# Kernel tuning notes

Measured on AMD Instinct MI355X. Metric: run time of the kernel, lower is better.

## Reference

```python
import jax, jax.numpy as jnp
import numpy as np

N_EMBD = 2048
N_HEAD = 16
HEAD_DIM = N_EMBD // N_HEAD
MAX_SEQ = 2048
ROPE_BASE = 10000.0


def _build_rope_cache(seq_len, head_dim, base):
    theta = 1.0 / (base ** (jnp.arange(0, head_dim, 2, dtype=jnp.float32) / head_dim))
    idx_theta = jnp.arange(seq_len, dtype=jnp.float32)[:, None] * theta[None, :]  # [T, hd/2]
    return jnp.cos(idx_theta), jnp.sin(idx_theta)


def _apply_rope(x, cos, sin):
    # x: [B, T, H, hd]; interleaved (even, odd) pairing along last dim
    B, T, H, hd = x.shape
    xf = x.astype(jnp.float32).reshape(B, T, H, hd // 2, 2)
    x0, x1 = xf[..., 0], xf[..., 1]
    c = cos[None, :T, None, :]
    s = sin[None, :T, None, :]
    out = jnp.stack([x0 * c - x1 * s, x1 * c + x0 * s], axis=-1)
    return out.reshape(B, T, H, hd).astype(x.dtype)


def setup_inputs() -> dict:
    key = jax.random.key(0)
    k1, k2, k3 = jax.random.split(key, 3)
    x = jax.random.normal(k1, (2, 2048, N_EMBD), dtype=jnp.float32)
    # torch Linear(D, 3D, bias=False): y = x @ W.T ; store as [D, 3D] for x @ W
    scale = 1.0 / np.sqrt(N_EMBD)
    w_attn = jax.random.normal(k2, (N_EMBD, 3 * N_EMBD), dtype=jnp.float32) * scale
    w_proj = jax.random.normal(k3, (N_EMBD, N_EMBD), dtype=jnp.float32) * scale
    return {"x": x, "w_attn": w_attn, "w_proj": w_proj}


def reference(x, w_attn, w_proj):
    B, T, D = x.shape
    cos, sin = _build_rope_cache(MAX_SEQ, HEAD_DIM, ROPE_BASE)
    qkv = x @ w_attn                                   # [B, T, 3D]
    q, k, v = jnp.split(qkv, 3, axis=-1)
    q = q.reshape(B, T, N_HEAD, HEAD_DIM)
    k = k.reshape(B, T, N_HEAD, HEAD_DIM)
    v = v.reshape(B, T, N_HEAD, HEAD_DIM)
    q = _apply_rope(q, cos, sin)
    k = _apply_rope(k, cos, sin)
    # non-causal SDPA (original calls F.sdpa without is_causal)
    scale = 1.0 / jnp.sqrt(jnp.asarray(HEAD_DIM, dtype=q.dtype))
    scores = jnp.einsum("bqhd,bkhd->bhqk", q, k) * scale
    attn = jax.nn.softmax(scores, axis=-1)
    y = jnp.einsum("bhqk,bkhd->bqhd", attn, v).reshape(B, T, D)
    return y @ w_proj
```

## Files before the change

kernel.cpp:

```cpp
#include <hip/hip_runtime.h>
#include <cstdint>
#include <cstddef>

typedef __attribute__((ext_vector_type(8))) short bf16x8;
typedef __attribute__((ext_vector_type(8))) unsigned short us8;
typedef __attribute__((ext_vector_type(4))) float f32x4;

#define TSEQ 2048

__device__ __forceinline__ unsigned short f2bf(float f) {
  union { float f; uint32_t u; } v; v.f = f;
  uint32_t u = v.u;
  uint32_t r = (u + 0x7FFFu + ((u >> 16) & 1u)) >> 16;
  return (unsigned short)r;
}
__device__ __forceinline__ unsigned short f2bf_trunc(float f) {
  union { float f; uint32_t u; } v; v.f = f;
  return (unsigned short)(v.u >> 16);
}
__device__ __forceinline__ float bf2f(unsigned short h) {
  union { uint32_t u; float f; } v; v.u = ((uint32_t)h) << 16;
  return v.f;
}

__device__ __forceinline__ void async16(const void* g, void* l) {
  __builtin_amdgcn_global_load_lds(
      (const __attribute__((address_space(1))) unsigned int*)g,
      (__attribute__((address_space(3))) unsigned int*)l,
      16, 0, 0);
}

__global__ __launch_bounds__(256) void rope_table(float2* __restrict__ tbl)
{
  const int idx = blockIdx.x * 256 + threadIdx.x;
  const int t = idx >> 6;
  const int j = idx & 63;
  float sn, cs;
  sincosf((float)t * exp2f((float)j * -0.2076205059273837f), &sn, &cs);
  tbl[idx] = make_float2(cs, sn);
}

__global__ __launch_bounds__(256) void cvt_x(
    const float* __restrict__ in, unsigned short* __restrict__ out)
{
  const size_t i = ((size_t)blockIdx.x * 256 + threadIdx.x) * 16;
  f32x4 a0 = *(const f32x4*)(in + i);
  f32x4 a1 = *(const f32x4*)(in + i + 4);
  f32x4 a2 = *(const f32x4*)(in + i + 8);
  f32x4 a3 = *(const f32x4*)(in + i + 12);
  us8 lo, hi;
#pragma unroll
  for (int j = 0; j < 4; j++) {
    lo[j] = f2bf(a0[j]); lo[j + 4] = f2bf(a1[j]);
    hi[j] = f2bf(a2[j]); hi[j + 4] = f2bf(a3[j]);
  }
  *(us8*)(out + i) = lo;
  *(us8*)(out + i + 8) = hi;
}

__global__ __launch_bounds__(256) void transpose_w(
    const float* __restrict__ in, unsigned short* __restrict__ out,
    int R, int C)
{
  __shared__ unsigned short tile[32][33];
  const int bx = blockIdx.x * 32;
  const int by = blockIdx.y * 32;
  const int tx = threadIdx.x & 31;
  const int ty = threadIdx.x >> 5;
#pragma unroll
  for (int r = ty; r < 32; r += 8)
    tile[r][tx] = f2bf(in[(size_t)(by + r) * C + bx + tx]);
  __syncthreads();
#pragma unroll
  for (int r = ty; r < 32; r += 8)
    out[(size_t)(bx + r) * R + by + tx] = tile[tx][r];
}

template <int MODE>
__global__ __launch_bounds__(256) void gemm_bt(
    const unsigned short* __restrict__ A,
    const unsigned short* __restrict__ Bt,
    void* __restrict__ Cv,
    int M, int N, int K, int ldc,
    const float2* __restrict__ tbl)
{
  __shared__ unsigned short As[2][128 * 32];
  __shared__ unsigned short Bs[2][128 * 32];
  const int tid  = threadIdx.x;
  const int lane = tid & 63;
  const int w    = tid >> 6;
  const int m0   = blockIdx.y * 128;
  const int n0   = blockIdx.x * 128;
  const int wm   = (w & 1) * 64;
  const int wn   = (w >> 1) * 64;

  const int srow = lane >> 2;
  const int scol = (lane & 3) * 8;
  const unsigned short* ga0 = A  + (size_t)(m0 + w * 16 + srow) * K + scol;
  const unsigned short* ga1 = ga0 + (size_t)64 * K;
  const unsigned short* gb0 = Bt + (size_t)(n0 + w * 16 + srow) * K + scol;
  const unsigned short* gb1 = gb0 + (size_t)64 * K;

  f32x4 acc[4][4];
#pragma unroll
  for (int i = 0; i < 4; i++)
#pragma unroll
    for (int j = 0; j < 4; j++) acc[i][j] = (f32x4){0.f, 0.f, 0.f, 0.f};

  const int frow = lane & 15;
  const int fcol = (lane >> 4) * 8;

  for (int kt = 0; kt < K; kt += 64) {
    __syncthreads();
    async16(ga0 + kt,      &As[0][w * 512]);
    async16(ga1 + kt,      &As[0][(4 + w) * 512]);
    async16(ga0 + kt + 32, &As[1][w * 512]);
    async16(ga1 + kt + 32, &As[1][(4 + w) * 512]);
    async16(gb0 + kt,      &Bs[0][w * 512]);
    async16(gb1 + kt,      &Bs[0][(4 + w) * 512]);
    async16(gb0 + kt + 32, &Bs[1][w * 512]);
    async16(gb1 + kt + 32, &Bs[1][(4 + w) * 512]);
    __syncthreads();

#pragma unroll
    for (int h = 0; h < 2; h++) {
      bf16x8 af[4], bfr[4];
#pragma unroll
      for (int i = 0; i < 4; i++)
        af[i] = *(const bf16x8*)&As[h][(wm + i * 16 + frow) * 32 + fcol];
#pragma unroll
      for (int i = 0; i < 4; i++)
        bfr[i] = *(const bf16x8*)&Bs[h][(wn + i * 16 + frow) * 32 + fcol];
#pragma unroll
      for (int mi = 0; mi < 4; mi++)
#pragma unroll
        for (int ni = 0; ni < 4; ni++)
          acc[mi][ni] = __builtin_amdgcn_mfma_f32_16x16x32_bf16(
              af[mi], bfr[ni], acc[mi][ni], 0, 0, 0);
    }
  }

  const int crow0 = m0 + wm + (lane >> 4) * 4;
  const int ccol0 = n0 + wn + (lane & 15);
  if (MODE == 1) {
    float* Cf = (float*)Cv;
#pragma unroll
    for (int mi = 0; mi < 4; mi++)
#pragma unroll
      for (int i = 0; i < 4; i++) {
        const int row = crow0 + mi * 16 + i;
#pragma unroll
        for (int ni = 0; ni < 4; ni++)
          Cf[(size_t)row * ldc + ccol0 + ni * 16] = acc[mi][ni][i];
      }
  } else {
    unsigned short* Cb = (unsigned short*)Cv;
    const bool doRope = (n0 < 4096);
    const float sc = (n0 < 2048) ? 0.08838834764831845f : 1.0f;
    const int odd = lane & 1;
#pragma unroll
    for (int mi = 0; mi < 4; mi++)
#pragma unroll
      for (int i = 0; i < 4; i++) {
        const int row = crow0 + mi * 16 + i;
        if (doRope) {
          const size_t tof = (size_t)(row & (TSEQ - 1)) * 64;
          float2 cs[4];
#pragma unroll
          for (int ni = 0; ni < 4; ni++)
            cs[ni] = tbl[tof + (((ccol0 + ni * 16) & 126) >> 1)];
#pragma unroll
          for (int ni = 0; ni < 4; ni++) {
            const float v = acc[mi][ni][i];
            const float p = __shfl_xor(v, 1);
            const float o = (odd ? (v * cs[ni].x + p * cs[ni].y)
                                 : (v * cs[ni].x - p * cs[ni].y)) * sc;
            Cb[(size_t)row * ldc + ccol0 + ni * 16] = f2bf(o);
          }
        } else {
#pragma unroll
          for (int ni = 0; ni < 4; ni++)
            Cb[(size_t)row * ldc + ccol0 + ni * 16] = f2bf(acc[mi][ni][i]);
        }
      }
  }
}

__global__ __launch_bounds__(256) void repack_v(
    const unsigned short* __restrict__ qkv, unsigned short* __restrict__ Vtg)
{
  __shared__ unsigned short tile[32][33];
  const int tt = blockIdx.x * 32;
  const int dd = blockIdx.y * 32;
  const int bh = blockIdx.z;
  const int b  = bh >> 4, h = bh & 15;
  const int tx = threadIdx.x & 31;
  const int ty = threadIdx.x >> 5;
#pragma unroll
  for (int r = ty; r < 32; r += 8)
    tile[r][tx] = qkv[(size_t)(b * TSEQ + tt + r) * 6144 + 4096 + h * 128 + dd + tx];
  __syncthreads();
#pragma unroll
  for (int r = ty; r < 32; r += 8)
    Vtg[(size_t)bh * 262144 + (size_t)(dd + r) * TSEQ + tt + tx] = tile[tx][r];
}

__global__ __launch_bounds__(256) void attn(
    const unsigned short* __restrict__ qkv,
    const unsigned short* __restrict__ Vtg,
    unsigned short* __restrict__ y)
{
  __shared__ unsigned short Ks[64 * 136];
  __shared__ unsigned short Vs[128 * 72];
  __shared__ unsigned short Ps[4][32 * 72];

  const int tid  = threadIdx.x;
  const int lane = tid & 63;
  const int w    = tid >> 6;
  const int q0   = blockIdx.x * 128;
  const int h    = blockIdx.y;
  const int b    = blockIdx.z;
  const int bh   = b * 16 + h;
  const int quad = lane >> 4;
  const int l15  = lane & 15;
  const int kq   = quad * 8;

  bf16x8 qa[2][4];
#pragma unroll
  for (int mt = 0; mt < 2; mt++) {
    const unsigned short* gQ =
        qkv + (size_t)(b * TSEQ + q0 + w * 32 + mt * 16 + l15) * 6144 + h * 128 + kq;
#pragma unroll
    for (int dc = 0; dc < 4; dc++) qa[mt][dc] = *(const bf16x8*)(gQ + dc * 32);
  }

  f32x4 ot[2][8];
#pragma unroll
  for (int mt = 0; mt < 2; mt++)
#pragma unroll
    for (int nt = 0; nt < 8; nt++) ot[mt][nt] = (f32x4){0.f, 0.f, 0.f, 0.f};
  float rs[2][4];
#pragma unroll
  for (int mt = 0; mt < 2; mt++)
#pragma unroll
    for (int i = 0; i < 4; i++) rs[mt][i] = 0.f;

  const int krow = tid >> 2;
  const int kd   = (tid & 3) * 32;
  const unsigned short* gK = qkv + (size_t)(b * TSEQ) * 6144 + 2048 + h * 128 + kd;
  const int vd = tid >> 1;
  const int vc = (tid & 1) * 32;
  const unsigned short* gVt = Vtg + (size_t)bh * 262144 + (size_t)vd * TSEQ + vc;

  us8 kreg[4], vreg[4];
  {
    const unsigned short* pk = gK + (size_t)krow * 6144;
#pragma unroll
    for (int j = 0; j < 4; j++) kreg[j] = *(const us8*)(pk + j * 8);
#pragma unroll
    for (int j = 0; j < 4; j++) vreg[j] = *(const us8*)(gVt + j * 8);
  }

  for (int kb = 0; kb < TSEQ; kb += 64) {
    __syncthreads();
#pragma unroll
    for (int j = 0; j < 4; j++)
      *(us8*)&Ks[krow * 136 + kd + j * 8] = kreg[j];
#pragma unroll
    for (int j = 0; j < 4; j++)
      *(us8*)&Vs[vd * 72 + vc + j * 8] = vreg[j];
    __syncthreads();

    if (kb + 64 < TSEQ) {
      const unsigned short* pk = gK + (size_t)(kb + 64 + krow) * 6144;
#pragma unroll
      for (int j = 0; j < 4; j++) kreg[j] = *(const us8*)(pk + j * 8);
      const unsigned short* pv = gVt + kb + 64;
#pragma unroll
      for (int j = 0; j < 4; j++) vreg[j] = *(const us8*)(pv + j * 8);
    }

    f32x4 s[2][4];
#pragma unroll
    for (int mt = 0; mt < 2; mt++)
#pragma unroll
      for (int ct = 0; ct < 4; ct++) s[mt][ct] = (f32x4){0.f, 0.f, 0.f, 0.f};
    __builtin_amdgcn_s_setprio(1);
#pragma unroll
    for (int dc = 0; dc < 4; dc++) {
#pragma unroll
      for (int ct = 0; ct < 4; ct++) {
        bf16x8 kf = *(const bf16x8*)&Ks[(ct * 16 + l15) * 136 + dc * 32 + kq];
        s[0][ct] = __builtin_amdgcn_mfma_f32_16x16x32_bf16(qa[0][dc], kf, s[0][ct], 0, 0, 0);
        s[1][ct] = __builtin_amdgcn_mfma_f32_16x16x32_bf16(qa[1][dc], kf, s[1][ct], 0, 0, 0);
      }
    }
    __builtin_amdgcn_s_setprio(0);

    unsigned short* pw = &Ps[w][0];
    float t8[2][4];
#pragma unroll
    for (int mt = 0; mt < 2; mt++)
#pragma unroll
      for (int i = 0; i < 4; i++) t8[mt][i] = 0.f;
#pragma unroll
    for (int mt = 0; mt < 2; mt++)
#pragma unroll
      for (int ct = 0; ct < 4; ct++)
#pragma unroll
        for (int i = 0; i < 4; i++) {
          const unsigned short us = f2bf_trunc(__expf(fminf(s[mt][ct][i], 30.f)));
          pw[(mt * 16 + quad * 4 + i) * 72 + ct * 16 + l15] = us;
          t8[mt][i] += bf2f(us);
        }
#pragma unroll
    for (int mt = 0; mt < 2; mt++)
#pragma unroll
      for (int i = 0; i < 4; i++) {
        float v = t8[mt][i];
        v += __shfl_xor(v, 1);
        v += __shfl_xor(v, 2);
        v += __shfl_xor(v, 4);
        v += __shfl_xor(v, 8);
        rs[mt][i] += v;
      }

    __asm__ volatile("s_waitcnt lgkmcnt(0)" ::: "memory");

    __builtin_amdgcn_s_setprio(1);
#pragma unroll
    for (int kc = 0; kc < 2; kc++) {
      bf16x8 pa0 = *(const bf16x8*)&pw[(l15) * 72 + kc * 32 + kq];
      bf16x8 pa1 = *(const bf16x8*)&pw[(16 + l15) * 72 + kc * 32 + kq];
#pragma unroll
      for (int nt = 0; nt < 8; nt++) {
        bf16x8 vb = *(const bf16x8*)&Vs[(nt * 16 + l15) * 72 + kc * 32 + kq];
        ot[0][nt] = __builtin_amdgcn_mfma_f32_16x16x32_bf16(pa0, vb, ot[0][nt], 0, 0, 0);
        ot[1][nt] = __builtin_amdgcn_mfma_f32_16x16x32_bf16(pa1, vb, ot[1][nt], 0, 0, 0);
      }
    }
    __builtin_amdgcn_s_setprio(0);
  }

#pragma unroll
  for (int mt = 0; mt < 2; mt++) {
    unsigned short* gy =
        y + (size_t)(b * TSEQ + q0 + w * 32 + mt * 16 + quad * 4) * 2048 + h * 128 + l15;
#pragma unroll
    for (int i = 0; i < 4; i++) {
      const float inv = 1.0f / rs[mt][i];
#pragma unroll
      for (int nt = 0; nt < 8; nt++)
        gy[(size_t)i * 2048 + nt * 16] = f2bf(ot[mt][nt][i] * inv);
    }
  }
}

extern "C" void kernel_launch(void* const* d_in, const int* in_sizes, int n_in,
                              void* d_out, int out_size, void* d_ws, size_t ws_size,
                              hipStream_t stream)
{
  const float* x      = (const float*)d_in[0];
  const float* w_attn = (const float*)d_in[1];
  const float* w_proj = (const float*)d_in[2];

  if (ws_size < 67108864u) return;

  char* ws = (char*)d_ws;
  unsigned short* qkv = (unsigned short*)(ws);
  unsigned short* xb  = (unsigned short*)(ws + 50331648);
  unsigned short* y   = xb;
  unsigned short* wT2 = (unsigned short*)(ws);
  unsigned short* wTa = (unsigned short*)d_out;
  float2* tbl = (float2*)((char*)d_out + 25165824);
  unsigned short* Vtg = (unsigned short*)d_out;

  transpose_w<<<dim3(192, 64), 256, 0, stream>>>(w_attn, wTa, 2048, 6144);
  rope_table<<<dim3(512), 256, 0, stream>>>(tbl);
  cvt_x<<<dim3(2048), 256, 0, stream>>>(x, xb);
  gemm_bt<2><<<dim3(48, 32), 256, 0, stream>>>(xb, wTa, (void*)qkv, 4096, 6144, 2048, 6144, tbl);
  repack_v<<<dim3(64, 4, 32), 256, 0, stream>>>(qkv, Vtg);
  attn<<<dim3(16, 16, 2), 256, 0, stream>>>(qkv, Vtg, y);
  transpose_w<<<dim3(64, 64), 256, 0, stream>>>(w_proj, wT2, 2048, 2048);
  gemm_bt<1><<<dim3(16, 32), 256, 0, stream>>>(y, wT2, d_out, 4096, 2048, 2048, 2048, nullptr);
}
```

Measured before the change: 453.9 us.

## Unfuse RoPE from QKV GEMM epilogue into standalone pass; vectorize V repack

Removes the precomputed rope table and the RoPE/scale epilogue from the QKV GEMM. A separate rope_qk kernel now reads Q and K back from the bf16 buffer, computes sin/cos inline and rewrites them in place. repack_v is rewritten to move 128-bit vectors through a larger padded tile. This simplifies the GEMM epilogue (no table loads or shuffles) at the cost of an extra read-write pass over Q and K, plus a second bf16 rounding before RoPE.

```diff
diff --git a/kernel.cpp b/kernel.cpp
--- a/kernel.cpp
+++ b/kernel.cpp
@@ -28,16 +28,6 @@
       (const __attribute__((address_space(1))) unsigned int*)g,
       (__attribute__((address_space(3))) unsigned int*)l,
       16, 0, 0);
-}
-
-__global__ __launch_bounds__(256) void rope_table(float2* __restrict__ tbl)
-{
-  const int idx = blockIdx.x * 256 + threadIdx.x;
-  const int t = idx >> 6;
-  const int j = idx & 63;
-  float sn, cs;
-  sincosf((float)t * exp2f((float)j * -0.2076205059273837f), &sn, &cs);
-  tbl[idx] = make_float2(cs, sn);
 }
 
 __global__ __launch_bounds__(256) void cvt_x(
@@ -76,13 +66,12 @@
     out[(size_t)(bx + r) * R + by + tx] = tile[tx][r];
 }
 
-template <int MODE>
+template <int CF32>
 __global__ __launch_bounds__(256) void gemm_bt(
     const unsigned short* __restrict__ A,
     const unsigned short* __restrict__ Bt,
     void* __restrict__ Cv,
-    int M, int N, int K, int ldc,
-    const float2* __restrict__ tbl)
+    int M, int N, int K, int ldc)
 {
   __shared__ unsigned short As[2][128 * 32];
   __shared__ unsigned short Bs[2][128 * 32];
@@ -142,7 +131,7 @@
 
   const int crow0 = m0 + wm + (lane >> 4) * 4;
   const int ccol0 = n0 + wn + (lane & 15);
-  if (MODE == 1) {
+  if (CF32) {
     float* Cf = (float*)Cv;
 #pragma unroll
     for (int mi = 0; mi < 4; mi++)
@@ -155,54 +144,75 @@
       }
   } else {
     unsigned short* Cb = (unsigned short*)Cv;
-    const bool doRope = (n0 < 4096);
-    const float sc = (n0 < 2048) ? 0.08838834764831845f : 1.0f;
-    const int odd = lane & 1;
 #pragma unroll
     for (int mi = 0; mi < 4; mi++)
 #pragma unroll
       for (int i = 0; i < 4; i++) {
         const int row = crow0 + mi * 16 + i;
-        if (doRope) {
-          const size_t tof = (size_t)(row & (TSEQ - 1)) * 64;
-          float2 cs[4];
-#pragma unroll
-          for (int ni = 0; ni < 4; ni++)
-            cs[ni] = tbl[tof + (((ccol0 + ni * 16) & 126) >> 1)];
-#pragma unroll
-          for (int ni = 0; ni < 4; ni++) {
-            const float v = acc[mi][ni][i];
-            const float p = __shfl_xor(v, 1);
-            const float o = (odd ? (v * cs[ni].x + p * cs[ni].y)
-                                 : (v * cs[ni].x - p * cs[ni].y)) * sc;
-            Cb[(size_t)row * ldc + ccol0 + ni * 16] = f2bf(o);
-          }
-        } else {
-#pragma unroll
-          for (int ni = 0; ni < 4; ni++)
-            Cb[(size_t)row * ldc + ccol0 + ni * 16] = f2bf(acc[mi][ni][i]);
-        }
-      }
-  }
+#pragma unroll
+        for (int ni = 0; ni < 4; ni++)
+          Cb[(size_t)row * ldc + ccol0 + ni * 16] = f2bf(acc[mi][ni][i]);
+      }
+  }
+}
+
+__global__ __launch_bounds__(256) void rope_qk(unsigned short* __restrict__ qkv)
+{
+  const int q   = blockIdx.x * 256 + threadIdx.x;
+  const int row = q >> 9;
+  const int cb  = (q & 511) * 8;
+  const int t   = row & (TSEQ - 1);
+  const int hd  = cb & 127;
+  const float sc = (cb < 2048) ? 0.08838834764831845f : 1.0f;
+  unsigned short* base = qkv + (size_t)row * 6144 + cb;
+  uint4 u = *(const uint4*)base;
+  uint32_t wd[4] = {u.x, u.y, u.z, u.w};
+#pragma unroll
+  for (int k = 0; k < 4; k++) {
+    const float theta = exp2f((float)(hd + 2 * k) * -0.1038102531f);
+    float s, c;
+    sincosf((float)t * theta, &s, &c);
+    const float x0 = bf2f((unsigned short)(wd[k] & 0xffffu));
+    const float x1 = bf2f((unsigned short)(wd[k] >> 16));
+    const float o0 = (x0 * c - x1 * s) * sc;
+    const float o1 = (x1 * c + x0 * s) * sc;
+    wd[k] = (uint32_t)f2bf(o0) | ((uint32_t)f2bf(o1) << 16);
+  }
+  *(uint4*)base = make_uint4(wd[0], wd[1], wd[2], wd[3]);
 }
 
 __global__ __launch_bounds__(256) void repack_v(
     const unsigned short* __restrict__ qkv, unsigned short* __restrict__ Vtg)
 {
-  __shared__ unsigned short tile[32][33];
-  const int tt = blockIdx.x * 32;
-  const int dd = blockIdx.y * 32;
-  const int bh = blockIdx.z;
+  __shared__ unsigned short tile[128][72];
+  const int tt = blockIdx.x * 64;
+  const int bh = blockIdx.y;
   const int b  = bh >> 4, h = bh & 15;
-  const int tx = threadIdx.x & 31;
-  const int ty = threadIdx.x >> 5;
-#pragma unroll
-  for (int r = ty; r < 32; r += 8)
-    tile[r][tx] = qkv[(size_t)(b * TSEQ + tt + r) * 6144 + 4096 + h * 128 + dd + tx];
+
+  {
+    const int r  = threadIdx.x & 63;
+    const int i0 = threadIdx.x >> 6;
+    const unsigned short* src =
+        qkv + (size_t)(b * TSEQ + tt + r) * 6144 + 4096 + h * 128;
+#pragma unroll
+    for (int i = i0; i < 16; i += 4) {
+      us8 v = *(const us8*)(src + i * 8);
+#pragma unroll
+      for (int k = 0; k < 8; k++) tile[i * 8 + k][r] = v[k];
+    }
+  }
   __syncthreads();
-#pragma unroll
-  for (int r = ty; r < 32; r += 8)
-    Vtg[(size_t)bh * 262144 + (size_t)(dd + r) * TSEQ + tt + tx] = tile[tx][r];
+  {
+    unsigned short* dst = Vtg + (size_t)bh * 262144 + tt;
+#pragma unroll
+    for (int it = 0; it < 4; it++) {
+      const int wdx = it * 256 + threadIdx.x;
+      const int d = wdx >> 3;
+      const int j = (wdx & 7) * 8;
+      us8 v = *(const us8*)&tile[d][j];
+      *(us8*)(dst + (size_t)d * TSEQ + j) = v;
+    }
+  }
 }
 
 __global__ __launch_bounds__(256) void attn(
@@ -372,15 +382,14 @@
   unsigned short* y   = xb;
   unsigned short* wT2 = (unsigned short*)(ws);
   unsigned short* wTa = (unsigned short*)d_out;
-  float2* tbl = (float2*)((char*)d_out + 25165824);
   unsigned short* Vtg = (unsigned short*)d_out;
 
   transpose_w<<<dim3(192, 64), 256, 0, stream>>>(w_attn, wTa, 2048, 6144);
-  rope_table<<<dim3(512), 256, 0, stream>>>(tbl);
   cvt_x<<<dim3(2048), 256, 0, stream>>>(x, xb);
-  gemm_bt<2><<<dim3(48, 32), 256, 0, stream>>>(xb, wTa, (void*)qkv, 4096, 6144, 2048, 6144, tbl);
-  repack_v<<<dim3(64, 4, 32), 256, 0, stream>>>(qkv, Vtg);
+  gemm_bt<0><<<dim3(48, 32), 256, 0, stream>>>(xb, wTa, (void*)qkv, 4096, 6144, 2048, 6144);
+  rope_qk<<<dim3(8192), 256, 0, stream>>>(qkv);
+  repack_v<<<dim3(32, 32), 256, 0, stream>>>(qkv, Vtg);
   attn<<<dim3(16, 16, 2), 256, 0, stream>>>(qkv, Vtg, y);
   transpose_w<<<dim3(64, 64), 256, 0, stream>>>(w_proj, wT2, 2048, 2048);
-  gemm_bt<1><<<dim3(16, 32), 256, 0, stream>>>(y, wT2, d_out, 4096, 2048, 2048, 2048, nullptr);
-}
+  gemm_bt<1><<<dim3(16, 32), 256, 0, stream>>>(y, wT2, d_out, 4096, 2048, 2048, 2048);
+}
```

After: 430.9 us. -5.1%, faster.
